# Performance work log

Hardware: AMD Instinct MI355X
Metric: run time of the kernel (lower is better)

## Reference

```python
import jax, jax.numpy as jnp
import numpy as np

B, L, H = 2, 512, 128

def setup_inputs() -> dict:
    key = jax.random.key(0)
    k1, k2, k3, _ = jax.random.split(key, 4)
    x = jax.random.normal(k1, (B, L, H), jnp.float32)
    y = jax.random.normal(k2, (B, L, H), jnp.float32)
    W_weight = jax.random.normal(k3, (H, 3 * H), jnp.float32) / np.sqrt(3 * H).astype(np.float32)
    W_bias = jnp.zeros((H,), jnp.float32)
    return {"x": x, "y": y, "W_weight": W_weight, "W_bias": W_bias}

def _span_max_context(x):
    """context[b,i,j,h] = max_{k=min(i,j)..max(i,j)} x[b,k,h], shape [B,L,L,H].
    Equivalent to the torch loop of diagonal running-max + symmetric scatter."""
    Bb, Ll, Hh = x.shape
    neg = jnp.full((Bb, 1, Hh), -jnp.inf, x.dtype)
    x_pad = jnp.concatenate([x, neg], axis=1)              # [B,L+1,H]
    d = jnp.arange(Ll)[:, None]                            # diagonal offset
    j = jnp.arange(Ll)[None, :]                            # start position
    shift_idx = jnp.minimum(d + j, Ll)                     # [L,L]; L -> -inf pad
    X2 = x_pad[:, shift_idx, :]                            # X2[b,d,j] = x[b,j+d]
    D = jax.lax.cummax(X2, axis=1)                         # D[b,d,j] = max_{k=j..j+d} x[b,k]
    i = jnp.arange(Ll)[:, None]
    jj = jnp.arange(Ll)[None, :]
    off = jnp.abs(i - jj)                                  # |i-j|
    lo = jnp.minimum(i, jj)                                # min(i,j)
    return D[:, off, lo, :]                                # [B,L,L,H]

def reference(x, y, W_weight, W_bias):
    Hh = x.shape[-1]
    ctx = _span_max_context(x)
    # Split W over the concat [x_i, y_j, context_ij] to avoid a [B,L,L,3H] intermediate.
    Wx, Wy, Wc = W_weight[:, :Hh], W_weight[:, Hh:2 * Hh], W_weight[:, 2 * Hh:]
    t = (jnp.einsum('blh,gh->blg', x, Wx)[:, :, None, :]
         + jnp.einsum('blh,gh->blg', y, Wy)[:, None, :, :]
         + jnp.einsum('bijh,gh->bijg', ctx, Wc)
         + W_bias)
    return jax.nn.gelu(t, approximate=False)               # [B,L,L,H]
```

## Files before the change

kernel.cpp:

```cpp
#include <hip/hip_runtime.h>
#include <hip/hip_bf16.h>

#define LL 512
#define HH 128
#define NBATCH 2
#define NT 32
#define NOFF (NT*(NT-1)/2)

typedef float f32x4 __attribute__((ext_vector_type(4)));
typedef short s16x8 __attribute__((ext_vector_type(8)));
typedef unsigned int u32x4 __attribute__((ext_vector_type(4)));

__device__ __forceinline__ unsigned short f2bfu(float f){
  __hip_bfloat16 h = __float2bfloat16(f);
  return __builtin_bit_cast(unsigned short, h);
}
__device__ __forceinline__ unsigned int bmax2(unsigned int a, unsigned int b){
  float lo = fmaxf(__uint_as_float(a << 16), __uint_as_float(b << 16));
  float hi = fmaxf(__uint_as_float(a & 0xFFFF0000u), __uint_as_float(b & 0xFFFF0000u));
  return __float_as_uint(hi) | (__float_as_uint(lo) >> 16);
}
__device__ __forceinline__ unsigned int packbf2(float lo, float hi){
  return ((__float_as_uint(hi) + 0x8000u) & 0xFFFF0000u)
       | ((__float_as_uint(lo) + 0x8000u) >> 16);
}
__device__ __forceinline__ u32x4 bmax4(u32x4 a, u32x4 b){
  u32x4 r; r[0]=bmax2(a[0],b[0]); r[1]=bmax2(a[1],b[1]);
  r[2]=bmax2(a[2],b[2]); r[3]=bmax2(a[3],b[3]); return r;
}
__device__ __forceinline__ float gelu_f(float v){
  float inner = v * fmaf(0.044715f, v*v, 1.0f);
  float e = __expf(1.5957691216f * inner);
  float s = __fdividef(1.0f, e + 1.0f);
  return fmaf(-v, s, v);
}
__device__ __forceinline__ f32x4 gelu4(f32x4 v){
  f32x4 r;
  #pragma unroll
  for (int i=0;i<4;++i) r[i] = gelu_f(v[i]);
  return r;
}

__global__ void prep_kernel(const float* __restrict__ x, const float* __restrict__ y,
                            const float* __restrict__ W, const float* __restrict__ bias,
                            float* __restrict__ t1, float* __restrict__ t2,
                            float* __restrict__ bmax, short* __restrict__ Wcb){
  int blk = blockIdx.x, tid = threadIdx.x;
  if (blk < NBATCH*LL){
    int b = blk >> 9, l = blk & (LL-1);
    __shared__ float xs[HH], ys[HH];
    size_t base = ((size_t)b*LL + l)*HH;
    if (tid < HH) xs[tid] = x[base + tid];
    else          ys[tid-HH] = y[base + tid - HH];
    __syncthreads();
    int role = tid >> 7, g = tid & (HH-1);
    const float4* wr = (const float4*)(W + (size_t)g*384 + role*HH);
    const float4* vs = (const float4*)(role ? ys : xs);
    float sA = 0.f, sB = 0.f;
    #pragma unroll
    for (int q=0;q<32;q+=2){
      float4 a = vs[q],   w1 = wr[q];
      sA = fmaf(a.x,w1.x, fmaf(a.y,w1.y, fmaf(a.z,w1.z, fmaf(a.w,w1.w, sA))));
      float4 c = vs[q+1], w2 = wr[q+1];
      sB = fmaf(c.x,w2.x, fmaf(c.y,w2.y, fmaf(c.z,w2.z, fmaf(c.w,w2.w, sB))));
    }
    float s = sA + sB;
    if (role == 0) t1[base + g] = s + bias[g];
    else           t2[base + g] = s;
  } else if (blk < NBATCH*LL + NBATCH*NT/2){
    int e = (blk - NBATCH*LL)*2 + (tid >> 7);
    int h = tid & (HH-1);
    int b = e >> 5, t = e & 31;
    float m = -INFINITY;
    #pragma unroll
    for (int r=0;r<16;++r) m = fmaxf(m, x[((size_t)b*LL + t*16 + r)*HH + h]);
    bmax[(size_t)e*HH + h] = m;
  } else {
    int e0 = ((blk - (NBATCH*LL + NBATCH*NT/2))*256 + tid)*8;
    #pragma unroll
    for (int i=0;i<8;++i){
      int e = e0 + i; int g = e >> 7, h = e & (HH-1);
      Wcb[e] = (short)f2bfu(W[(size_t)g*384 + 256 + h]);
    }
  }
}

__global__ __launch_bounds__(256, 4) void ctx_kernel(
    const float* __restrict__ x, const float* __restrict__ t1,
    const float* __restrict__ t2, const float* __restrict__ bmax,
    const short* __restrict__ Wcb, float* __restrict__ out)
{
  __shared__ __align__(16) unsigned short shs[8192];
  const int tid = threadIdx.x;
  const int b = blockIdx.y;
  const int w = tid >> 6, l = tid & 63, l16 = l & 15, lhi = l >> 4;
  const size_t bL = (size_t)b*LL;

  if (blockIdx.x < NOFF) {
    int ti = 0, tj;
    { int rem = blockIdx.x;
      while (rem >= NT-1-ti){ rem -= NT-1-ti; ++ti; }
      tj = ti + 1 + rem; }

    unsigned short* sfxU = shs;
    unsigned short* pfgU = shs + 2048;
    { int role = tid >> 7, h = tid & (HH-1);
      if (role == 0){
        const float* xp = x + (bL + ti*16)*HH + h;
        float run = -INFINITY;
        #pragma unroll
        for (int r=15;r>=0;--r){ run = fmaxf(run, xp[r*HH]);
          sfxU[r*HH + (h ^ ((r&7)<<3))] = f2bfu(run); }
      } else {
        const float* bp = bmax + ((size_t)b*NT)*HH + h;
        float run = -INFINITY;
        for (int t=ti+1; t<tj; ++t) run = fmaxf(run, bp[t*HH]);
        const float* xp = x + (bL + tj*16)*HH + h;
        #pragma unroll
        for (int r=0;r<16;++r){ run = fmaxf(run, xp[r*HH]);
          pfgU[r*HH + (h ^ ((r&7)<<3))] = f2bfu(run); }
      }
    }
    __syncthreads();

    const int qrow = tj*16 + l16;
    const size_t qoff = (bL + qrow)*HH;

    #pragma unroll
    for (int ph=0; ph<2; ++ph){
      const int pt0 = w*4 + ph*2, pt1 = pt0 + 1;
      u32x4 fr0[4], fr1[4];
      #pragma unroll
      for (int kb=0;kb<4;++kb){
        int h0 = kb*32 + lhi*8;
        u32x4 p  = *(const u32x4*)&pfgU[l16*HH + (h0 ^ ((l16&7)<<3))];
        u32x4 s0 = *(const u32x4*)&sfxU[pt0*HH + (h0 ^ ((pt0&7)<<3))];
        u32x4 s1 = *(const u32x4*)&sfxU[pt1*HH + (h0 ^ ((pt1&7)<<3))];
        fr0[kb] = bmax4(s0, p);
        fr1[kb] = bmax4(s1, p);
      }
      const size_t i0off = (bL + ti*16 + pt0)*HH;
      const size_t i1off = (bL + ti*16 + pt1)*HH;
      const size_t o1r0 = ((bL + ti*16 + pt0)*LL + qrow)*HH;
      const size_t o1r1 = ((bL + ti*16 + pt1)*LL + qrow)*HH;
      const size_t o2r0 = ((bL + qrow)*LL + ti*16 + pt0)*HH;
      const size_t o2r1 = o2r0 + HH;

      #pragma unroll
      for (int nt=0; nt<8; ++nt){
        const int gg = nt*16 + l16;
        s16x8 wcf[4];
        #pragma unroll
        for (int kb=0;kb<4;++kb)
          wcf[kb] = *(const s16x8*)(Wcb + (size_t)gg*HH + kb*32 + lhi*8);
        f32x4 a0 = (f32x4){0.f,0.f,0.f,0.f}, a1 = a0;
        #pragma unroll
        for (int kb=0;kb<4;++kb){
          a0 = __builtin_amdgcn_mfma_f32_16x16x32_bf16(wcf[kb],
                 __builtin_bit_cast(s16x8, fr0[kb]), a0, 0, 0, 0);
          a1 = __builtin_amdgcn_mfma_f32_16x16x32_bf16(wcf[kb],
                 __builtin_bit_cast(s16x8, fr1[kb]), a1, 0, 0, 0);
        }
        const int g0 = nt*16 + lhi*4;
        f32x4 t1j = *(const f32x4*)(t1 + qoff + g0);
        f32x4 t2j = *(const f32x4*)(t2 + qoff + g0);
        f32x4 t1i0 = *(const f32x4*)(t1 + i0off + g0);
        f32x4 t2i0 = *(const f32x4*)(t2 + i0off + g0);
        f32x4 t1i1 = *(const f32x4*)(t1 + i1off + g0);
        f32x4 t2i1 = *(const f32x4*)(t2 + i1off + g0);
        *(f32x4*)(out + o1r0 + g0) = gelu4(a0 + t1i0 + t2j);
        *(f32x4*)(out + o2r0 + g0) = gelu4(a0 + t1j + t2i0);
        *(f32x4*)(out + o1r1 + g0) = gelu4(a1 + t1i1 + t2j);
        *(f32x4*)(out + o2r1 + g0) = gelu4(a1 + t1j + t2i1);
      }
    }
  } else {
    const int td = blockIdx.x - NOFF;
    unsigned short* M = shs;
    { int e = tid*8; int r = e >> 7, h0 = e & (HH-1);
      const float* xp = x + (bL + td*16 + r)*HH + h0;
      f32x4 v0 = *(const f32x4*)xp, v1 = *(const f32x4*)(xp+4);
      u32x4 pk; pk[0]=packbf2(v0[0],v0[1]); pk[1]=packbf2(v0[2],v0[3]);
      pk[2]=packbf2(v1[0],v1[1]); pk[3]=packbf2(v1[2],v1[3]);
      *(u32x4*)&M[r*HH + (h0 ^ ((r&7)<<3))] = pk;
    }
    __syncthreads();
    #pragma unroll
    for (int k=1;k<4;++k){
      int e = tid*8; int r = e >> 7, h0 = e & (HH-1);
      int r2 = min(r + (1<<(k-1)), 15);
      u32x4 a = *(const u32x4*)&M[((k-1)*16 + r )*HH + (h0 ^ ((r &7)<<3))];
      u32x4 c = *(const u32x4*)&M[((k-1)*16 + r2)*HH + (h0 ^ ((r2&7)<<3))];
      *(u32x4*)&M[(k*16 + r)*HH + (h0 ^ ((r&7)<<3))] = bmax4(a, c);
      __syncthreads();
    }

    const int qrow = td*16 + l16;
    const size_t qoff = (bL + qrow)*HH;

    #pragma unroll
    for (int ph=0; ph<2; ++ph){
      const int ptA = w*4 + ph*2;
      u32x4 fr[2][4];
      #pragma unroll
      for (int pi=0; pi<2; ++pi){
        int pt = ptA + pi;
        int a = min(pt, l16), bb = max(pt, l16);
        int len = bb - a + 1;
        int k = 31 - __clz(len); if (k > 3) k = 3;
        int r2 = bb + 1 - (1 << k);
        #pragma unroll
        for (int kb=0;kb<4;++kb){
          int h0 = kb*32 + lhi*8;
          u32x4 ua = *(const u32x4*)&M[(k*16 + a )*HH + (h0 ^ ((a &7)<<3))];
          u32x4 ub = *(const u32x4*)&M[(k*16 + r2)*HH + (h0 ^ ((r2&7)<<3))];
          fr[pi][kb] = bmax4(ua, ub);
        }
      }
      const int pt0 = ptA, pt1 = ptA + 1;
      const size_t i0off = (bL + td*16 + pt0)*HH;
      const size_t i1off = (bL + td*16 + pt1)*HH;
      const size_t o0 = ((bL + td*16 + pt0)*LL + qrow)*HH;
      const size_t o1 = ((bL + td*16 + pt1)*LL + qrow)*HH;

      #pragma unroll
      for (int nt=0; nt<8; ++nt){
        const int gg = nt*16 + l16;
        s16x8 wcf[4];
        #pragma unroll
        for (int kb=0;kb<4;++kb)
          wcf[kb] = *(const s16x8*)(Wcb + (size_t)gg*HH + kb*32 + lhi*8);
        f32x4 a0 = (f32x4){0.f,0.f,0.f,0.f}, a1 = a0;
        #pragma unroll
        for (int kb=0;kb<4;++kb){
          a0 = __builtin_amdgcn_mfma_f32_16x16x32_bf16(wcf[kb],
                 __builtin_bit_cast(s16x8, fr[0][kb]), a0, 0, 0, 0);
          a1 = __builtin_amdgcn_mfma_f32_16x16x32_bf16(wcf[kb],
                 __builtin_bit_cast(s16x8, fr[1][kb]), a1, 0, 0, 0);
        }
        const int g0 = nt*16 + lhi*4;
        f32x4 t2j = *(const f32x4*)(t2 + qoff + g0);
        f32x4 t1i0 = *(const f32x4*)(t1 + i0off + g0);
        f32x4 t1i1 = *(const f32x4*)(t1 + i1off + g0);
        *(f32x4*)(out + o0 + g0) = gelu4(a0 + t1i0 + t2j);
        *(f32x4*)(out + o1 + g0) = gelu4(a1 + t1i1 + t2j);
      }
    }
  }
}

extern "C" void kernel_launch(void* const* d_in, const int* in_sizes, int n_in,
                              void* d_out, int out_size, void* d_ws, size_t ws_size,
                              hipStream_t stream) {
  const float* x    = (const float*)d_in[0];
  const float* y    = (const float*)d_in[1];
  const float* W    = (const float*)d_in[2];
  const float* bias = (const float*)d_in[3];
  float* out = (float*)d_out;

  float* t1 = (float*)d_ws;
  float* t2 = t1 + (size_t)NBATCH*LL*HH;
  float* bmax = t2 + (size_t)NBATCH*LL*HH;
  short* Wcb = (short*)(bmax + (size_t)NBATCH*NT*HH);

  prep_kernel<<<NBATCH*LL + NBATCH*NT/2 + 8, 256, 0, stream>>>(x, y, W, bias, t1, t2, bmax, Wcb);
  ctx_kernel<<<dim3(NOFF + NT, NBATCH), 256, 0, stream>>>(x, t1, t2, bmax, Wcb, out);
}
```

Before: 100.6 us.

## Transpose MFMA results through per-wave LDS for coalesced output stores

MFMA accumulators are now written to a per-wave LDS staging buffer with an XOR swizzle, then read back so that each group of 8 lanes stores a contiguous 128-byte segment along the hidden dimension. Before, each lane stored 16 bytes into a different output row. The change also merges the diagonal and off-diagonal tile paths into one epilogue, and widens shared memory to hold the staging buffers. The aim is better write coalescing on this store-bound kernel, at the cost of extra LDS traffic and more shared memory per block, which may lower occupancy.

```diff
diff --git a/kernel.cpp b/kernel.cpp
--- a/kernel.cpp
+++ b/kernel.cpp
@@ -90,95 +90,45 @@
     const float* __restrict__ t2, const float* __restrict__ bmax,
     const short* __restrict__ Wcb, float* __restrict__ out)
 {
-  __shared__ __align__(16) unsigned short shs[8192];
+  __shared__ __align__(16) unsigned int shs[8192];
   const int tid = threadIdx.x;
   const int b = blockIdx.y;
   const int w = tid >> 6, l = tid & 63, l16 = l & 15, lhi = l >> 4;
   const size_t bL = (size_t)b*LL;
-
-  if (blockIdx.x < NOFF) {
-    int ti = 0, tj;
-    { int rem = blockIdx.x;
-      while (rem >= NT-1-ti){ rem -= NT-1-ti; ++ti; }
-      tj = ti + 1 + rem; }
-
-    unsigned short* sfxU = shs;
-    unsigned short* pfgU = shs + 2048;
-    { int role = tid >> 7, h = tid & (HH-1);
-      if (role == 0){
-        const float* xp = x + (bL + ti*16)*HH + h;
-        float run = -INFINITY;
-        #pragma unroll
-        for (int r=15;r>=0;--r){ run = fmaxf(run, xp[r*HH]);
-          sfxU[r*HH + (h ^ ((r&7)<<3))] = f2bfu(run); }
-      } else {
-        const float* bp = bmax + ((size_t)b*NT)*HH + h;
-        float run = -INFINITY;
-        for (int t=ti+1; t<tj; ++t) run = fmaxf(run, bp[t*HH]);
-        const float* xp = x + (bL + tj*16)*HH + h;
-        #pragma unroll
-        for (int r=0;r<16;++r){ run = fmaxf(run, xp[r*HH]);
-          pfgU[r*HH + (h ^ ((r&7)<<3))] = f2bfu(run); }
-      }
+  float* Bw = (float*)shs + w*1024;
+  unsigned short* sIU = (unsigned short*)(shs + 4096);
+  unsigned short* sJU = sIU + 2048;
+  unsigned short* M   = (unsigned short*)(shs + 4096);
+
+  const bool isdiag = (blockIdx.x >= NOFF);
+  int ti, tj;
+  if (!isdiag){
+    int rem = blockIdx.x; ti = 0;
+    while (rem >= NT-1-ti){ rem -= NT-1-ti; ++ti; }
+    tj = ti + 1 + rem;
+  } else { ti = tj = blockIdx.x - NOFF; }
+
+  if (!isdiag){
+    int role = tid >> 7, h = tid & (HH-1);
+    if (role == 0){
+      const float* xp = x + (bL + ti*16)*HH + h;
+      float run = -INFINITY;
+      #pragma unroll
+      for (int r=15;r>=0;--r){ run = fmaxf(run, xp[r*HH]);
+        sIU[r*HH + (h ^ ((r&7)<<3))] = f2bfu(run); }
+    } else {
+      const float* bp = bmax + ((size_t)b*NT)*HH + h;
+      float run = -INFINITY;
+      for (int t=ti+1;t<tj;++t) run = fmaxf(run, bp[t*HH]);
+      const float* xp = x + (bL + tj*16)*HH + h;
+      #pragma unroll
+      for (int r=0;r<16;++r){ run = fmaxf(run, xp[r*HH]);
+        sJU[r*HH + (h ^ ((r&7)<<3))] = f2bfu(run); }
     }
     __syncthreads();
-
-    const int qrow = tj*16 + l16;
-    const size_t qoff = (bL + qrow)*HH;
-
-    #pragma unroll
-    for (int ph=0; ph<2; ++ph){
-      const int pt0 = w*4 + ph*2, pt1 = pt0 + 1;
-      u32x4 fr0[4], fr1[4];
-      #pragma unroll
-      for (int kb=0;kb<4;++kb){
-        int h0 = kb*32 + lhi*8;
-        u32x4 p  = *(const u32x4*)&pfgU[l16*HH + (h0 ^ ((l16&7)<<3))];
-        u32x4 s0 = *(const u32x4*)&sfxU[pt0*HH + (h0 ^ ((pt0&7)<<3))];
-        u32x4 s1 = *(const u32x4*)&sfxU[pt1*HH + (h0 ^ ((pt1&7)<<3))];
-        fr0[kb] = bmax4(s0, p);
-        fr1[kb] = bmax4(s1, p);
-      }
-      const size_t i0off = (bL + ti*16 + pt0)*HH;
-      const size_t i1off = (bL + ti*16 + pt1)*HH;
-      const size_t o1r0 = ((bL + ti*16 + pt0)*LL + qrow)*HH;
-      const size_t o1r1 = ((bL + ti*16 + pt1)*LL + qrow)*HH;
-      const size_t o2r0 = ((bL + qrow)*LL + ti*16 + pt0)*HH;
-      const size_t o2r1 = o2r0 + HH;
-
-      #pragma unroll
-      for (int nt=0; nt<8; ++nt){
-        const int gg = nt*16 + l16;
-        s16x8 wcf[4];
-        #pragma unroll
-        for (int kb=0;kb<4;++kb)
-          wcf[kb] = *(const s16x8*)(Wcb + (size_t)gg*HH + kb*32 + lhi*8);
-        f32x4 a0 = (f32x4){0.f,0.f,0.f,0.f}, a1 = a0;
-        #pragma unroll
-        for (int kb=0;kb<4;++kb){
-          a0 = __builtin_amdgcn_mfma_f32_16x16x32_bf16(wcf[kb],
-                 __builtin_bit_cast(s16x8, fr0[kb]), a0, 0, 0, 0);
-          a1 = __builtin_amdgcn_mfma_f32_16x16x32_bf16(wcf[kb],
-                 __builtin_bit_cast(s16x8, fr1[kb]), a1, 0, 0, 0);
-        }
-        const int g0 = nt*16 + lhi*4;
-        f32x4 t1j = *(const f32x4*)(t1 + qoff + g0);
-        f32x4 t2j = *(const f32x4*)(t2 + qoff + g0);
-        f32x4 t1i0 = *(const f32x4*)(t1 + i0off + g0);
-        f32x4 t2i0 = *(const f32x4*)(t2 + i0off + g0);
-        f32x4 t1i1 = *(const f32x4*)(t1 + i1off + g0);
-        f32x4 t2i1 = *(const f32x4*)(t2 + i1off + g0);
-        *(f32x4*)(out + o1r0 + g0) = gelu4(a0 + t1i0 + t2j);
-        *(f32x4*)(out + o2r0 + g0) = gelu4(a0 + t1j + t2i0);
-        *(f32x4*)(out + o1r1 + g0) = gelu4(a1 + t1i1 + t2j);
-        *(f32x4*)(out + o2r1 + g0) = gelu4(a1 + t1j + t2i1);
-      }
-    }
   } else {
-    const int td = blockIdx.x - NOFF;
-    unsigned short* M = shs;
     { int e = tid*8; int r = e >> 7, h0 = e & (HH-1);
-      const float* xp = x + (bL + td*16 + r)*HH + h0;
+      const float* xp = x + (bL + ti*16 + r)*HH + h0;
       f32x4 v0 = *(const f32x4*)xp, v1 = *(const f32x4*)(xp+4);
       u32x4 pk; pk[0]=packbf2(v0[0],v0[1]); pk[1]=packbf2(v0[2],v0[3]);
       pk[2]=packbf2(v1[0],v1[1]); pk[3]=packbf2(v1[2],v1[3]);
@@ -194,42 +144,53 @@
       *(u32x4*)&M[(k*16 + r)*HH + (h0 ^ ((r&7)<<3))] = bmax4(a, c);
       __syncthreads();
     }
-
-    const int qrow = td*16 + l16;
-    const size_t qoff = (bL + qrow)*HH;
-
-    #pragma unroll
-    for (int ph=0; ph<2; ++ph){
-      const int ptA = w*4 + ph*2;
-      u32x4 fr[2][4];
-      #pragma unroll
-      for (int pi=0; pi<2; ++pi){
-        int pt = ptA + pi;
-        int a = min(pt, l16), bb = max(pt, l16);
-        int len = bb - a + 1;
-        int k = 31 - __clz(len); if (k > 3) k = 3;
-        int r2 = bb + 1 - (1 << k);
+  }
+
+  const int i0 = ti*16, j0 = tj*16;
+
+  #pragma unroll
+  for (int ps=0; ps<2; ++ps){
+    const int ptA = w*4 + ps*2;
+    u32x4 fr[2][4];
+    if (!isdiag){
+      #pragma unroll
+      for (int s=0;s<2;++s){
+        int pt = ptA + s;
         #pragma unroll
         for (int kb=0;kb<4;++kb){
           int h0 = kb*32 + lhi*8;
-          u32x4 ua = *(const u32x4*)&M[(k*16 + a )*HH + (h0 ^ ((a &7)<<3))];
-          u32x4 ub = *(const u32x4*)&M[(k*16 + r2)*HH + (h0 ^ ((r2&7)<<3))];
-          fr[pi][kb] = bmax4(ua, ub);
-        }
-      }
-      const int pt0 = ptA, pt1 = ptA + 1;
-      const size_t i0off = (bL + td*16 + pt0)*HH;
-      const size_t i1off = (bL + td*16 + pt1)*HH;
-      const size_t o0 = ((bL + td*16 + pt0)*LL + qrow)*HH;
-      const size_t o1 = ((bL + td*16 + pt1)*LL + qrow)*HH;
-
-      #pragma unroll
-      for (int nt=0; nt<8; ++nt){
-        const int gg = nt*16 + l16;
+          u32x4 si = *(const u32x4*)&sIU[pt*HH + (h0 ^ ((pt&7)<<3))];
+          u32x4 pj = *(const u32x4*)&sJU[l16*HH + (h0 ^ ((l16&7)<<3))];
+          fr[s][kb] = bmax4(si, pj);
+        }
+      }
+    } else {
+      #pragma unroll
+      for (int s=0;s<2;++s){
+        int pt = ptA + s;
+        int a = min(pt, l16), bb2 = max(pt, l16);
+        int len = bb2 - a + 1;
+        int k = 31 - __clz(len); if (k>3) k=3;
+        int r2 = bb2 + 1 - (1<<k);
+        #pragma unroll
+        for (int kb=0;kb<4;++kb){
+          int h0 = kb*32 + lhi*8;
+          u32x4 ua = *(const u32x4*)&M[(k*16+a )*HH + (h0 ^ ((a &7)<<3))];
+          u32x4 ub = *(const u32x4*)&M[(k*16+r2)*HH + (h0 ^ ((r2&7)<<3))];
+          fr[s][kb] = bmax4(ua, ub);
+        }
+      }
+    }
+
+    #pragma unroll
+    for (int q4=0; q4<4; ++q4){
+      #pragma unroll
+      for (int hf=0; hf<2; ++hf){
+        const int nt = q4*2 + hf;
         s16x8 wcf[4];
         #pragma unroll
         for (int kb=0;kb<4;++kb)
-          wcf[kb] = *(const s16x8*)(Wcb + (size_t)gg*HH + kb*32 + lhi*8);
+          wcf[kb] = *(const s16x8*)(Wcb + (size_t)(nt*16+l16)*HH + kb*32 + lhi*8);
         f32x4 a0 = (f32x4){0.f,0.f,0.f,0.f}, a1 = a0;
         #pragma unroll
         for (int kb=0;kb<4;++kb){
@@ -238,13 +199,38 @@
           a1 = __builtin_amdgcn_mfma_f32_16x16x32_bf16(wcf[kb],
                  __builtin_bit_cast(s16x8, fr[1][kb]), a1, 0, 0, 0);
         }
-        const int g0 = nt*16 + lhi*4;
-        f32x4 t2j = *(const f32x4*)(t2 + qoff + g0);
-        f32x4 t1i0 = *(const f32x4*)(t1 + i0off + g0);
-        f32x4 t1i1 = *(const f32x4*)(t1 + i1off + g0);
-        *(f32x4*)(out + o0 + g0) = gelu4(a0 + t1i0 + t2j);
-        *(f32x4*)(out + o1 + g0) = gelu4(a1 + t1i1 + t2j);
-      }
+        const int wo = (hf*16 + lhi*4) ^ ((l16&7)<<2);
+        *(f32x4*)&Bw[      l16*32 + wo] = a0;
+        *(f32x4*)&Bw[512 + l16*32 + wo] = a1;
+      }
+      asm volatile("" ::: "memory");
+
+      const int gq = q4*32 + (l&7)*4;
+      #pragma unroll
+      for (int s=0;s<2;++s){
+        const int irow = i0 + ptA + s;
+        f32x4 t1i = *(const f32x4*)(t1 + (bL+irow)*HH + gq);
+        #pragma unroll
+        for (int it=0; it<2; ++it){
+          const int j = it*8 + (l>>3);
+          f32x4 v = *(const f32x4*)&Bw[s*512 + j*32 + (((l&7)*4) ^ ((j&7)<<2))];
+          f32x4 t2j = *(const f32x4*)(t2 + (bL+j0+j)*HH + gq);
+          *(f32x4*)(out + ((bL+irow)*LL + j0+j)*HH + gq) = gelu4(v + t1i + t2j);
+        }
+      }
+      if (!isdiag){
+        const int s2 = (l>>3)&1;
+        const int icol = i0 + ptA + s2;
+        f32x4 t2i = *(const f32x4*)(t2 + (bL+icol)*HH + gq);
+        #pragma unroll
+        for (int it=0; it<4; ++it){
+          const int j = it*4 + (l>>4);
+          f32x4 v = *(const f32x4*)&Bw[s2*512 + j*32 + (((l&7)*4) ^ ((j&7)<<2))];
+          f32x4 t1j = *(const f32x4*)(t1 + (bL+j0+j)*HH + gq);
+          *(f32x4*)(out + ((bL+j0+j)*LL + icol)*HH + gq) = gelu4(v + t1j + t2i);
+        }
+      }
+      asm volatile("" ::: "memory");
     }
   }
 }
```

After: 98.00 us. -2.5%, faster.
